# Kernel tuning notes

Measured on AMD Instinct MI355X. Metric: run time of the kernel, lower is better.

Reference implementation:

```python
import jax, jax.numpy as jnp
import numpy as np

BLUR = 0.05
P = 2
EPS_FINAL = BLUR ** P          # geomloss: eps = blur**p = 0.0025
DIAMETER = 2.0                 # max cosine cost magnitude
SCALING = 0.5                  # geomloss default; eps decays by scaling**p per step
N_FINAL_ITERS = 4              # extra balancing iterations at the final eps


def eps_schedule():
    eps_list = []
    e = DIAMETER ** P
    while e > EPS_FINAL:
        eps_list.append(e)
        e = e * (SCALING ** P)
    eps_list.extend([EPS_FINAL] * N_FINAL_ITERS)
    return eps_list


def cosine_cost(a, b):
    # a: (N, D), b: (M, D) -> (N, M) cost = 1 - cos_sim
    an = a / (jnp.linalg.norm(a, axis=1, keepdims=True) + 1e-12)
    bn = b / (jnp.linalg.norm(b, axis=1, keepdims=True) + 1e-12)
    return 1.0 - an @ bn.T


def softmin(C, pot, log_w, eps):
    # -eps * LSE_j( log_w + (pot_j - C_ij)/eps ) ; C: (N, M), pot: (M,)
    return -eps * jax.nn.logsumexp(log_w + (pot[None, :] - C) / eps, axis=1)


def sinkhorn_divergence(Cxy, Cxx, Cyy):
    N, M = Cxy.shape
    log_a = -jnp.log(jnp.asarray(N, dtype=Cxy.dtype))  # uniform weights
    log_b = -jnp.log(jnp.asarray(M, dtype=Cxy.dtype))
    sg = jax.lax.stop_gradient
    # Sinkhorn iterations run on detached costs (geomloss envelope-theorem trick)
    Cxy_s, Cxx_s, Cyy_s = sg(Cxy), sg(Cxx), sg(Cyy)
    f = jnp.zeros((N,), Cxy.dtype)
    g = jnp.zeros((M,), Cxy.dtype)
    fxx = jnp.zeros((N,), Cxy.dtype)
    gyy = jnp.zeros((M,), Cxy.dtype)
    for eps in eps_schedule():
        # symmetric (debiasing) potentials: averaged fixed-point update
        fxx = 0.5 * (fxx + softmin(Cxx_s, fxx, log_a, eps))
        gyy = 0.5 * (gyy + softmin(Cyy_s, gyy, log_b, eps))
        # cross potentials: simultaneous (Jacobi) update
        f, g = softmin(Cxy_s, g, log_b, eps), softmin(Cxy_s.T, f, log_a, eps)
    # final extrapolation step with gradients flowing through the costs
    eps = EPS_FINAL
    f_fin = softmin(Cxy, sg(g), log_b, eps)
    g_fin = softmin(Cxy.T, sg(f), log_a, eps)
    fxx_fin = softmin(Cxx, sg(fxx), log_a, eps)
    gyy_fin = softmin(Cyy, sg(gyy), log_b, eps)
    return jnp.mean(f_fin - fxx_fin) + jnp.mean(g_fin - gyy_fin)


def setup_inputs() -> dict:
    key = jax.random.key(0)
    k1, k2, k3 = jax.random.split(key, 3)
    x1 = jax.random.normal(k1, (8192, 256), dtype=jnp.float32)
    x2 = jax.random.normal(k2, (8192, 256), dtype=jnp.float32)
    w = jax.random.uniform(k3, (256,), dtype=jnp.float32)
    return {"x1": x1, "x2": x2, "w": w}


def reference(x1, x2, w):
    # Dist_loss.forward: clamp+renormalize learned per-feature weights, scale x1
    w_c = jnp.clip(w, 0.0, 2.0)
    w_c = w_c / jnp.mean(w_c)
    a = w_c[None, :] * x1
    Cxy = cosine_cost(a, x2)
    Cxx = cosine_cost(a, a)
    Cyy = cosine_cost(x2, x2)
    return sinkhorn_divergence(Cxy, Cxx, Cyy)
```

## Files before the change

kernel.cpp:

```cpp
#include <hip/hip_runtime.h>
#include <math.h>

#define N 8192
#define D 256
#define LN2 0.6931471805599453f
#define LDSROW 280
#define TSLOTS 1152

typedef short short8 __attribute__((ext_vector_type(8)));
typedef float f32x16 __attribute__((ext_vector_type(16)));
typedef unsigned short ushort;

__device__ __forceinline__ float fexp2(float x) { return __builtin_amdgcn_exp2f(x); }
__device__ __forceinline__ float flog2(float x) { return __builtin_amdgcn_logf(x); }

__device__ __forceinline__ ushort bf16r(float x) {
    unsigned int u = __float_as_uint(x);
    return (ushort)((u + 0x7FFF + ((u >> 16) & 1)) >> 16);
}

__device__ __forceinline__ void gl_lds16(const ushort* g, ushort* l) {
    __builtin_amdgcn_global_load_lds(
        (const __attribute__((address_space(1))) unsigned int*)g,
        (__attribute__((address_space(3))) unsigned int*)l, 16, 0, 0);
}

__global__ void prep_wc(const float* __restrict__ w, float* __restrict__ wc) {
    int t = threadIdx.x;
    float v = fminf(fmaxf(w[t], 0.0f), 2.0f);
    float s = v;
#pragma unroll
    for (int m = 1; m < 64; m <<= 1) s += __shfl_xor(s, m);
    __shared__ float sm[4];
    if ((t & 63) == 0) sm[t >> 6] = s;
    __syncthreads();
    float mean = (sm[0] + sm[1] + sm[2] + sm[3]) * (1.0f / 256.0f);
    wc[t] = v / mean;
}

__global__ void prep_normalize(const float* __restrict__ x1, const float* __restrict__ x2,
                               const float* __restrict__ wc,
                               ushort* __restrict__ an_i, ushort* __restrict__ bn_i) {
    int row = blockIdx.x;
    int t = threadIdx.x;
    int r; float v; ushort* ip;
    if (row < N) { r = row;     v = x1[(size_t)r * D + t] * wc[t]; ip = an_i; }
    else         { r = row - N; v = x2[(size_t)r * D + t];         ip = bn_i; }
    float ss = v * v;
#pragma unroll
    for (int m = 1; m < 64; m <<= 1) ss += __shfl_xor(ss, m);
    __shared__ float sm[4];
    if ((t & 63) == 0) sm[t >> 6] = ss;
    __syncthreads();
    float denom = sqrtf(sm[0] + sm[1] + sm[2] + sm[3]) + 1e-12f;
    ip[(size_t)r * D + t] = bf16r(v / denom);
}

__global__ void init_pots(float* __restrict__ pots, float* __restrict__ potm1) {
    int id = blockIdx.x * 256 + threadIdx.x;
    pots[id] = 0.0f;
    potm1[id] = -1.0f;
}

__global__ __launch_bounds__(256, 2) void softmin_mfma(
    const ushort* __restrict__ an_i, const ushort* __restrict__ bn_i,
    const float* __restrict__ potm1,
    float2* __restrict__ parts, float k1) {
    int bx = blockIdx.x;
    int k = bx & 7;
    int q = bx >> 3;
    int task = k >> 1;
    int split = ((k & 1) << 1) | (q & 1);
    int rb = q >> 1;
    const ushort* jp = (task == 0 || task == 3) ? an_i : bn_i;
    const ushort* ip = (task == 0 || task == 2) ? an_i : bn_i;
    const float* pm1 = potm1 + (size_t)task * N;

    int t = threadIdx.x;
    int wave = t >> 6, lane = t & 63;
    int l31 = lane & 31, lh = lane >> 5;
    int i0 = rb * 256 + wave * 64;

    __shared__ ushort lbuf[2][TSLOTS * 8];

    short8 bi0[16], bi1[16];
    {
        const ushort* ib = ip + (size_t)(i0 + l31) * D + lh * 8;
#pragma unroll
        for (int c = 0; c < 16; ++c) {
            bi0[c] = *(const short8*)(ib + c * 16);
            bi1[c] = *(const short8*)(ib + (size_t)32 * D + c * 16);
        }
    }
#pragma unroll
    for (int c = 0; c < 16; ++c) {
        asm volatile("" : "+a"(bi0[c]), "+a"(bi1[c]));
    }

    const int jbase0 = split * 2048;

    auto stage = [&](int b, int js) {
        const ushort* gb = jp + (size_t)(jbase0 + js * 32) * D;
        ushort* lb = &lbuf[b][0];
#pragma unroll
        for (int r = 0; r < 5; ++r) {
            if (r == 4 && t >= 128) break;
            int s = r * 256 + t;
            int row = s / 35;
            int c = s - row * 35;
            row = row > 31 ? 31 : row;
            c = c > 31 ? 31 : c;
            gl_lds16(gb + row * D + c * 8, lb + s * 8);
        }
    };

    float m0 = -INFINITY, s0 = 0.0f, m1 = -INFINITY, s1 = 0.0f;

    stage(0, 0);
    for (int js = 0; js < 64; ++js) {
        int cur = js & 1;
        __syncthreads();
        if (js < 63) stage(cur ^ 1, js + 1);

        int j0 = jbase0 + js * 32;
        float pjk[16];
#pragma unroll
        for (int g = 0; g < 4; ++g) {
            float4 pv = *(const float4*)&pm1[j0 + 8 * g + 4 * lh];
            pjk[4 * g + 0] = pv.x * k1; pjk[4 * g + 1] = pv.y * k1;
            pjk[4 * g + 2] = pv.z * k1; pjk[4 * g + 3] = pv.w * k1;
        }

        const ushort* lrow = &lbuf[cur][l31 * LDSROW + lh * 8];
        f32x16 acc0 = {}; f32x16 acc1 = {};
#pragma unroll
        for (int c = 0; c < 16; ++c) {
            short8 af = *(const short8*)(lrow + c * 16);
            acc0 = __builtin_amdgcn_mfma_f32_32x32x16_bf16(af, bi0[c], acc0, 0, 0, 0);
            acc1 = __builtin_amdgcn_mfma_f32_32x32x16_bf16(af, bi1[c], acc1, 0, 0, 0);
        }

        {
            float tv[16];
#pragma unroll
            for (int r = 0; r < 16; ++r) tv[r] = fmaf(acc0[r], k1, pjk[r]);
            float tm = tv[0];
#pragma unroll
            for (int r = 1; r < 16; ++r) tm = fmaxf(tm, tv[r]);
            float mn = fmaxf(m0, tm);
            float ad = 0.0f;
#pragma unroll
            for (int r = 0; r < 16; ++r) ad += fexp2(tv[r] - mn);
            s0 = s0 * fexp2(m0 - mn) + ad; m0 = mn;
        }
        {
            float tv[16];
#pragma unroll
            for (int r = 0; r < 16; ++r) tv[r] = fmaf(acc1[r], k1, pjk[r]);
            float tm = tv[0];
#pragma unroll
            for (int r = 1; r < 16; ++r) tm = fmaxf(tm, tv[r]);
            float mn = fmaxf(m1, tm);
            float ad = 0.0f;
#pragma unroll
            for (int r = 0; r < 16; ++r) ad += fexp2(tv[r] - mn);
            s1 = s1 * fexp2(m1 - mn) + ad; m1 = mn;
        }
    }
    float mo = __shfl_xor(m0, 32), so = __shfl_xor(s0, 32);
    float M0 = fmaxf(m0, mo);
    float S0 = s0 * fexp2(m0 - M0) + so * fexp2(mo - M0);
    mo = __shfl_xor(m1, 32); so = __shfl_xor(s1, 32);
    float M1 = fmaxf(m1, mo);
    float S1 = s1 * fexp2(m1 - M1) + so * fexp2(mo - M1);
    if (lane < 32) {
        size_t r0 = (size_t)task * N + (i0 + l31);
        size_t r1 = r0 + 32;
        parts[r0 * 4 + split] = make_float2(M0, S0);
        parts[r1 * 4 + split] = make_float2(M1, S1);
    }
}

__global__ void merge_pots(const float2* __restrict__ parts, float* __restrict__ pots,
                           float* __restrict__ potm1, float eps, float logw, int do_avg) {
    int id = blockIdx.x * 256 + threadIdx.x;
    int task = id >> 13;
    int row = id & (N - 1);
    const float2* p = parts + (size_t)id * 4;
    float2 a = p[0], b = p[1], c = p[2], d = p[3];
    float M = fmaxf(fmaxf(a.x, b.x), fmaxf(c.x, d.x));
    float S = a.y * fexp2(a.x - M) + b.y * fexp2(b.x - M) +
              c.y * fexp2(c.x - M) + d.y * fexp2(d.x - M);
    float lse = LN2 * (M + flog2(S));
    float v = -eps * (logw + lse);
    if (do_avg && task < 2) v = 0.5f * (pots[id] + v);
    pots[id] = v;
    int ct = (task < 2) ? task : (5 - task);
    potm1[(size_t)ct * N + row] = v - 1.0f;
}

__global__ void final_reduce(const float* __restrict__ pots, float* __restrict__ out) {
    int t = threadIdx.x;
    float s = 0.0f;
    for (int i = t; i < N; i += 256)
        s += (pots[2 * N + i] - pots[i]) + (pots[3 * N + i] - pots[N + i]);
#pragma unroll
    for (int m = 1; m < 64; m <<= 1) s += __shfl_xor(s, m);
    __shared__ float sm[4];
    if ((t & 63) == 0) sm[t >> 6] = s;
    __syncthreads();
    if (t == 0) out[0] = (sm[0] + sm[1] + sm[2] + sm[3]) * (1.0f / (float)N);
}

extern "C" void kernel_launch(void* const* d_in, const int* in_sizes, int n_in,
                              void* d_out, int out_size, void* d_ws, size_t ws_size,
                              hipStream_t stream) {
    const float* x1 = (const float*)d_in[0];
    const float* x2 = (const float*)d_in[1];
    const float* w  = (const float*)d_in[2];
    float* out = (float*)d_out;

    ushort* an_i = (ushort*)d_ws;
    ushort* bn_i = an_i + (size_t)N * D;
    float*  wc   = (float*)(bn_i + (size_t)N * D);
    float*  pots = wc + 256;
    float*  potm1 = pots + 4 * N;
    float2* parts = (float2*)(potm1 + 4 * N);

    prep_wc<<<1, 256, 0, stream>>>(w, wc);
    prep_normalize<<<2 * N, 256, 0, stream>>>(x1, x2, wc, an_i, bn_i);
    init_pots<<<4 * N / 256, 256, 0, stream>>>(pots, potm1);

    const float eps_list[10] = {4.0f, 1.0f, 0.25f, 0.0625f, 0.015625f,
                                0.00390625f, 0.0025f, 0.0025f, 0.0025f, 0.0025f};
    const float logw = -logf((float)N);
    const float LOG2E = 1.4426950408889634f;
    for (int it = 0; it < 10; ++it) {
        softmin_mfma<<<512, 256, 0, stream>>>(an_i, bn_i, potm1, parts, LOG2E / eps_list[it]);
        merge_pots<<<4 * N / 256, 256, 0, stream>>>(parts, pots, potm1,
                                                    eps_list[it], logw, 1);
    }
    softmin_mfma<<<512, 256, 0, stream>>>(an_i, bn_i, potm1, parts, LOG2E / 0.0025f);
    merge_pots<<<4 * N / 256, 256, 0, stream>>>(parts, pots, potm1, 0.0025f, logw, 0);
    final_reduce<<<1, 256, 0, stream>>>(pots, out);
}
```

Before: 1.662 ms.

## Stage 64-row tiles with XOR-swizzled LDS layout and tree-reduced epilogue

The j-tile staged per barrier grows from 32 to 64 rows, so the loop does half as many __syncthreads, and each stage is processed as two 32-row MFMA sub-blocks. The padded LDS layout (35 slots per row with clamped duplicate loads) is replaced by a dense 256-element row layout with an XOR swizzle on the 16-byte chunk index, which avoids bank conflicts without wasting loads. The softmin epilogue now uses tree reductions for the max and the sum to shorten dependency chains. LDS use per block roughly doubles (64 KB), which may limit the two-blocks-per-CU occupancy target.

```diff
diff --git a/kernel.cpp b/kernel.cpp
--- a/kernel.cpp
+++ b/kernel.cpp
@@ -4,8 +4,6 @@
 #define N 8192
 #define D 256
 #define LN2 0.6931471805599453f
-#define LDSROW 280
-#define TSLOTS 1152
 
 typedef short short8 __attribute__((ext_vector_type(8)));
 typedef float f32x16 __attribute__((ext_vector_type(16)));
@@ -79,9 +77,10 @@
     int t = threadIdx.x;
     int wave = t >> 6, lane = t & 63;
     int l31 = lane & 31, lh = lane >> 5;
+    int xk = l31 & 7;
     int i0 = rb * 256 + wave * 64;
 
-    __shared__ ushort lbuf[2][TSLOTS * 8];
+    __shared__ ushort lbuf[2][2048 * 8];
 
     short8 bi0[16], bi1[16];
     {
@@ -99,72 +98,70 @@
 
     const int jbase0 = split * 2048;
 
-    auto stage = [&](int b, int js) {
-        const ushort* gb = jp + (size_t)(jbase0 + js * 32) * D;
-        ushort* lb = &lbuf[b][0];
-#pragma unroll
-        for (int r = 0; r < 5; ++r) {
-            if (r == 4 && t >= 128) break;
+    auto stage = [&](int b, int iv) {
+        const ushort* gb = jp + (size_t)(jbase0 + iv * 64) * D;
+        ushort* lbp = &lbuf[b][0];
+#pragma unroll
+        for (int r = 0; r < 8; ++r) {
             int s = r * 256 + t;
-            int row = s / 35;
-            int c = s - row * 35;
-            row = row > 31 ? 31 : row;
-            c = c > 31 ? 31 : c;
-            gl_lds16(gb + row * D + c * 8, lb + s * 8);
+            int row = s >> 5;
+            int c = s & 31;
+            int csrc = c ^ (row & 7);
+            gl_lds16(gb + (size_t)row * D + csrc * 8, lbp + s * 8);
         }
     };
 
     float m0 = -INFINITY, s0 = 0.0f, m1 = -INFINITY, s1 = 0.0f;
 
+    auto epi = [&](const f32x16& acc, const float* pj, float& mR, float& sR) {
+        float tv[16];
+#pragma unroll
+        for (int r = 0; r < 16; ++r) tv[r] = fmaf(acc[r], k1, pj[r]);
+        float x0 = fmaxf(tv[0], tv[1]),  x1 = fmaxf(tv[2], tv[3]),
+              x2 = fmaxf(tv[4], tv[5]),  x3 = fmaxf(tv[6], tv[7]),
+              x4 = fmaxf(tv[8], tv[9]),  x5 = fmaxf(tv[10], tv[11]),
+              x6 = fmaxf(tv[12], tv[13]), x7 = fmaxf(tv[14], tv[15]);
+        float y0 = fmaxf(x0, x1), y1 = fmaxf(x2, x3),
+              y2 = fmaxf(x4, x5), y3 = fmaxf(x6, x7);
+        float tm = fmaxf(fmaxf(y0, y1), fmaxf(y2, y3));
+        float mn = fmaxf(mR, tm);
+        float e[16];
+#pragma unroll
+        for (int r = 0; r < 16; ++r) e[r] = fexp2(tv[r] - mn);
+        float sA = (e[0] + e[1]) + (e[2] + e[3]),   sB = (e[4] + e[5]) + (e[6] + e[7]),
+              sC = (e[8] + e[9]) + (e[10] + e[11]), sD = (e[12] + e[13]) + (e[14] + e[15]);
+        float ad = (sA + sB) + (sC + sD);
+        sR = fmaf(sR, fexp2(mR - mn), ad);
+        mR = mn;
+    };
+
     stage(0, 0);
-    for (int js = 0; js < 64; ++js) {
-        int cur = js & 1;
+    for (int iv = 0; iv < 32; ++iv) {
+        int cur = iv & 1;
         __syncthreads();
-        if (js < 63) stage(cur ^ 1, js + 1);
-
-        int j0 = jbase0 + js * 32;
-        float pjk[16];
-#pragma unroll
-        for (int g = 0; g < 4; ++g) {
-            float4 pv = *(const float4*)&pm1[j0 + 8 * g + 4 * lh];
-            pjk[4 * g + 0] = pv.x * k1; pjk[4 * g + 1] = pv.y * k1;
-            pjk[4 * g + 2] = pv.z * k1; pjk[4 * g + 3] = pv.w * k1;
-        }
-
-        const ushort* lrow = &lbuf[cur][l31 * LDSROW + lh * 8];
-        f32x16 acc0 = {}; f32x16 acc1 = {};
-#pragma unroll
-        for (int c = 0; c < 16; ++c) {
-            short8 af = *(const short8*)(lrow + c * 16);
-            acc0 = __builtin_amdgcn_mfma_f32_32x32x16_bf16(af, bi0[c], acc0, 0, 0, 0);
-            acc1 = __builtin_amdgcn_mfma_f32_32x32x16_bf16(af, bi1[c], acc1, 0, 0, 0);
-        }
-
-        {
-            float tv[16];
-#pragma unroll
-            for (int r = 0; r < 16; ++r) tv[r] = fmaf(acc0[r], k1, pjk[r]);
-            float tm = tv[0];
-#pragma unroll
-            for (int r = 1; r < 16; ++r) tm = fmaxf(tm, tv[r]);
-            float mn = fmaxf(m0, tm);
-            float ad = 0.0f;
-#pragma unroll
-            for (int r = 0; r < 16; ++r) ad += fexp2(tv[r] - mn);
-            s0 = s0 * fexp2(m0 - mn) + ad; m0 = mn;
-        }
-        {
-            float tv[16];
-#pragma unroll
-            for (int r = 0; r < 16; ++r) tv[r] = fmaf(acc1[r], k1, pjk[r]);
-            float tm = tv[0];
-#pragma unroll
-            for (int r = 1; r < 16; ++r) tm = fmaxf(tm, tv[r]);
-            float mn = fmaxf(m1, tm);
-            float ad = 0.0f;
-#pragma unroll
-            for (int r = 0; r < 16; ++r) ad += fexp2(tv[r] - mn);
-            s1 = s1 * fexp2(m1 - mn) + ad; m1 = mn;
+        if (iv < 31) stage(cur ^ 1, iv + 1);
+
+#pragma unroll
+        for (int u = 0; u < 2; ++u) {
+            int j0 = jbase0 + iv * 64 + u * 32;
+            float pjk[16];
+#pragma unroll
+            for (int g = 0; g < 4; ++g) {
+                float4 pv = *(const float4*)&pm1[j0 + 8 * g + 4 * lh];
+                pjk[4 * g + 0] = pv.x * k1; pjk[4 * g + 1] = pv.y * k1;
+                pjk[4 * g + 2] = pv.z * k1; pjk[4 * g + 3] = pv.w * k1;
+            }
+            const ushort* lb = &lbuf[cur][(u * 32 + l31) * 256];
+            f32x16 acc0 = {}; f32x16 acc1 = {};
+#pragma unroll
+            for (int c = 0; c < 16; ++c) {
+                int sl = (2 * c + lh) ^ xk;
+                short8 af = *(const short8*)(lb + sl * 8);
+                acc0 = __builtin_amdgcn_mfma_f32_32x32x16_bf16(af, bi0[c], acc0, 0, 0, 0);
+                acc1 = __builtin_amdgcn_mfma_f32_32x32x16_bf16(af, bi1[c], acc1, 0, 0, 0);
+            }
+            epi(acc0, pjk, m0, s0);
+            epi(acc1, pjk, m1, s1);
         }
     }
     float mo = __shfl_xor(m0, 32), so = __shfl_xor(s0, 32);
```

Measured after the change: 1.798 ms. +8.2%, slower.
